# Performance work log

Hardware: AMD Instinct MI355X
Metric: run time of the kernel (lower is better)

Reference implementation:

```python
import jax, jax.numpy as jnp
import numpy as np

T = 100          # number of landscape sample points
K_MAX = 2        # landscape depth
GRID = (256, 256)
N = GRID[0] * GRID[1]
B = 256          # batch size
P = 1024         # persistence pairs per sample (from the cubical complex)
DIMENSIONS = (0, 1)
BIG = jnp.float32(1e30)  # finite sentinel instead of inf (avoids inf arithmetic)


def setup_inputs() -> dict:
    key = jax.random.key(0)
    k1, k2, k3, k4 = jax.random.split(key, 4)
    inputs = jax.random.uniform(k1, (B, N), dtype=jnp.float32)
    dim_idx = jax.random.randint(k2, (B, P), 0, 2, dtype=jnp.int32)
    b_loc = jax.random.randint(k3, (B, P), 0, N, dtype=jnp.int32)
    d_loc = jax.random.randint(k4, (B, P), 0, N, dtype=jnp.int32)
    # persistence pairs satisfy death value >= birth value; swap to honor that
    vb = jnp.take_along_axis(inputs, b_loc, axis=1)
    vd = jnp.take_along_axis(inputs, d_loc, axis=1)
    swap = vb > vd
    birth_loc = jnp.where(swap, d_loc, b_loc)
    death_loc = jnp.where(swap, b_loc, d_loc)
    return {"inputs": inputs, "dim_idx": dim_idx,
            "birth_loc": birth_loc, "death_loc": death_loc}


def _landscape_sample(dtm, dim_idx, b_loc, d_loc):
    # dtm: [N] filtration values; pairs: [P] each
    births = dtm[b_loc]  # [P] birth value = input at birth cell
    deaths = dtm[d_loc]  # [P]
    lands, trange = [], []
    for dim in DIMENSIONS:
        valid = dim_idx == dim                     # [P] pairs of this homology dim
        count = jnp.sum(valid)
        # robust t-range: first K_MAX valid pairs in given (lexsort) order
        rank = jnp.cumsum(valid.astype(jnp.int32)) - 1
        sel = valid & (rank < K_MAX)
        t_min = jnp.min(jnp.where(sel, births, BIG))
        t_max = jnp.max(jnp.where(sel, deaths, -BIG))
        t_min = jnp.where(count > 0, t_min, 0.0)
        t_max = jnp.where(count > 0, t_max, 0.0)
        # original custom grad does NOT differentiate through tseq
        tseq = jax.lax.stop_gradient(jnp.linspace(t_min, t_max, T))  # [T]
        b = jnp.where(valid, births, BIG)
        d = jnp.where(valid, deaths, -BIG)
        # tent functions: [T, P]
        fab = jnp.maximum(jnp.minimum(tseq[:, None] - b[None, :],
                                      d[None, :] - tseq[:, None]), 0.0)
        land, _ = jax.lax.top_k(fab, K_MAX)        # == -sort(-fab)[:, :K_MAX]
        land = jnp.where(count > 0, land, jnp.zeros_like(land))
        nonzero = (count > 0) & (jnp.max(land) > 0)
        trange.append(jnp.where(nonzero, t_min, 0.0))
        trange.append(jnp.where(nonzero, t_max, 0.0))
        lands.append(land)
    return jnp.stack(lands), jax.lax.stop_gradient(jnp.stack(trange))


def reference(inputs, dim_idx, birth_loc, death_loc):
    # landscape: [B, len(DIMENSIONS), T, K_MAX]; t_range: [B, 2*len(DIMENSIONS)]
    land, t_range = jax.vmap(_landscape_sample)(inputs, dim_idx, birth_loc, death_loc)
    return land, t_range
```

## Files before the change

kernel.cpp:

```cpp
#include <hip/hip_runtime.h>

#define TT 100
#define PP 1024
#define NN 65536
#define BIGV 1e30f

__global__ __launch_bounds__(1024, 8) void adpl_kernel(
    const float* __restrict__ inputs,
    const int*   __restrict__ dim_idx,
    const int*   __restrict__ birth_loc,
    const int*   __restrict__ death_loc,
    float*       __restrict__ out_land,
    float*       __restrict__ out_trange)
{
    __shared__ float2 bd[PP];
    __shared__ unsigned long long s_mask[16];
    __shared__ float  s_tmin, s_tmax;
    __shared__ int    s_count;
    __shared__ int    s_maxland;
    __shared__ float2 s_part[TT][9];

    const int b   = blockIdx.x;
    const int d   = blockIdx.y;
    const int tid = threadIdx.x;

    if (tid == 0) s_maxland = 0;

    {
        const int p  = tid;
        const int di = dim_idx [(size_t)b * PP + p];
        const int bl = birth_loc[(size_t)b * PP + p];
        const int dl = death_loc[(size_t)b * PP + p];
        const float bv = inputs[(size_t)b * NN + bl];
        const float dv = inputs[(size_t)b * NN + dl];
        const bool v = (di == d);
        bd[p] = v ? make_float2(bv, dv) : make_float2(BIGV, -BIGV);
        const unsigned long long m = __ballot(v);
        if ((tid & 63) == 0) s_mask[tid >> 6] = m;
    }
    __syncthreads();

    if (tid == 0) {
        int cnt = 0, p1 = -1, p2 = -1;
        for (int w = 0; w < 16; w++) {
            unsigned long long m = s_mask[w];
            cnt += __popcll(m);
            if (p2 < 0 && m) {
                if (p1 < 0) {
                    p1 = w * 64 + __ffsll(m) - 1;
                    m &= m - 1;
                    if (m) p2 = w * 64 + __ffsll(m) - 1;
                } else {
                    p2 = w * 64 + __ffsll(m) - 1;
                }
            }
        }
        float tmin = 0.f, tmax = 0.f;
        if (cnt > 0) {
            const float2 e1 = bd[p1];
            tmin = e1.x; tmax = e1.y;
            if (cnt > 1) {
                const float2 e2 = bd[p2];
                tmin = fminf(tmin, e2.x);
                tmax = fmaxf(tmax, e2.y);
            }
        }
        s_tmin = tmin; s_tmax = tmax; s_count = cnt;
    }
    __syncthreads();

    {
        const int t = tid >> 3;
        const int c = tid & 7;
        if (t < TT) {
            const float tmin = s_tmin, tmax = s_tmax;
            const float step = (tmax - tmin) * (1.0f / (TT - 1));
            const float tv = (t == TT - 1) ? tmax : fmaf((float)t, step, tmin);
            float M1 = 0.f, M2 = 0.f;
            #pragma unroll 8
            for (int i = 0; i < 128; i++) {
                const float2 e = bd[8 * i + c];
                const float f = fminf(tv - e.x, e.y - tv);
                M2 = fmaxf(M2, fminf(M1, f));
                M1 = fmaxf(M1, f);
            }
            s_part[t][c] = make_float2(M1, M2);
        }
    }
    __syncthreads();

    if (tid < TT) {
        const int t = tid;
        float m1 = 0.f, m2 = 0.f;
        #pragma unroll
        for (int cc = 0; cc < 8; cc++) {
            const float2 pr = s_part[t][cc];
            m2 = fmaxf(m2, fminf(m1, pr.x));
            m1 = fmaxf(m1, pr.x);
            m2 = fmaxf(m2, pr.y);
        }
        const size_t base = ((size_t)(b * 2 + d) * TT + t) * 2;
        out_land[base + 0] = m1;
        out_land[base + 1] = m2;
        atomicMax(&s_maxland, __float_as_int(m1));
    }
    __syncthreads();

    if (tid == 0) {
        const bool nz = (s_count > 0) && (__int_as_float(s_maxland) > 0.f);
        out_trange[(size_t)b * 4 + 2 * d + 0] = nz ? s_tmin : 0.f;
        out_trange[(size_t)b * 4 + 2 * d + 1] = nz ? s_tmax : 0.f;
    }
}

extern "C" void kernel_launch(void* const* d_in, const int* in_sizes, int n_in,
                              void* d_out, int out_size, void* d_ws, size_t ws_size,
                              hipStream_t stream) {
    const float* inputs    = (const float*)d_in[0];
    const int*   dim_idx   = (const int*)d_in[1];
    const int*   birth_loc = (const int*)d_in[2];
    const int*   death_loc = (const int*)d_in[3];

    const int B = in_sizes[1] / PP;

    float* out_land   = (float*)d_out;
    float* out_trange = out_land + (size_t)B * 2 * TT * 2;

    dim3 grid(B, 2);
    adpl_kernel<<<grid, 1024, 0, stream>>>(inputs, dim_idx, birth_loc, death_loc,
                                           out_land, out_trange);
}
```

Measured before the change: 105.4 us.

## Register-block four t-values per thread and predicate gathers on dimension match

The tent-function top-2 pass is remapped so each thread handles 4 sample points across 32 pair lanes instead of 1 point across 8 lanes. Each shared-memory pair load is now reused four times, and the final reduction grows to 32 partials per t. Birth and death locations and input values are only gathered for pairs whose dimension matches, which roughly halves scattered global reads. Output stores are vectorised to float2. In exchange, only 800 threads do the main loop and the reduction is longer.

```diff
diff --git a/kernel.cpp b/kernel.cpp
--- a/kernel.cpp
+++ b/kernel.cpp
@@ -18,7 +18,7 @@
     __shared__ float  s_tmin, s_tmax;
     __shared__ int    s_count;
     __shared__ int    s_maxland;
-    __shared__ float2 s_part[TT][9];
+    __shared__ float2 s_part[TT][33];
 
     const int b   = blockIdx.x;
     const int d   = blockIdx.y;
@@ -28,13 +28,16 @@
 
     {
         const int p  = tid;
-        const int di = dim_idx [(size_t)b * PP + p];
-        const int bl = birth_loc[(size_t)b * PP + p];
-        const int dl = death_loc[(size_t)b * PP + p];
-        const float bv = inputs[(size_t)b * NN + bl];
-        const float dv = inputs[(size_t)b * NN + dl];
+        const int di = dim_idx[(size_t)b * PP + p];
         const bool v = (di == d);
-        bd[p] = v ? make_float2(bv, dv) : make_float2(BIGV, -BIGV);
+        float bv = BIGV, dv = -BIGV;
+        if (v) {
+            const int bl = birth_loc[(size_t)b * PP + p];
+            const int dl = death_loc[(size_t)b * PP + p];
+            bv = inputs[(size_t)b * NN + bl];
+            dv = inputs[(size_t)b * NN + dl];
+        }
+        bd[p] = make_float2(bv, dv);
         const unsigned long long m = __ballot(v);
         if ((tid & 63) == 0) s_mask[tid >> 6] = m;
     }
@@ -69,47 +72,55 @@
     }
     __syncthreads();
 
-    {
-        const int t = tid >> 3;
-        const int c = tid & 7;
-        if (t < TT) {
-            const float tmin = s_tmin, tmax = s_tmax;
-            const float step = (tmax - tmin) * (1.0f / (TT - 1));
-            const float tv = (t == TT - 1) ? tmax : fmaf((float)t, step, tmin);
-            float M1 = 0.f, M2 = 0.f;
-            #pragma unroll 8
-            for (int i = 0; i < 128; i++) {
-                const float2 e = bd[8 * i + c];
-                const float f = fminf(tv - e.x, e.y - tv);
-                M2 = fmaxf(M2, fminf(M1, f));
-                M1 = fmaxf(M1, f);
+    if (tid < 800) {
+        const int tg = tid >> 5;
+        const int c  = tid & 31;
+        const float tmin = s_tmin, tmax = s_tmax;
+        const float step = (tmax - tmin) * (1.0f / (TT - 1));
+        float tv[4], m1[4], m2[4];
+        #pragma unroll
+        for (int j = 0; j < 4; j++) {
+            const int t = 4 * tg + j;
+            tv[j] = (t == TT - 1) ? tmax : fmaf((float)t, step, tmin);
+            m1[j] = 0.f; m2[j] = 0.f;
+        }
+        #pragma unroll 8
+        for (int i = 0; i < 32; i++) {
+            const float2 e = bd[32 * i + c];
+            #pragma unroll
+            for (int j = 0; j < 4; j++) {
+                const float f = fminf(tv[j] - e.x, e.y - tv[j]);
+                m2[j] = fmaxf(m2[j], fminf(m1[j], f));
+                m1[j] = fmaxf(m1[j], f);
             }
-            s_part[t][c] = make_float2(M1, M2);
         }
+        #pragma unroll
+        for (int j = 0; j < 4; j++)
+            s_part[4 * tg + j][c] = make_float2(m1[j], m2[j]);
     }
     __syncthreads();
 
     if (tid < TT) {
         const int t = tid;
         float m1 = 0.f, m2 = 0.f;
-        #pragma unroll
-        for (int cc = 0; cc < 8; cc++) {
-            const float2 pr = s_part[t][cc];
-            m2 = fmaxf(m2, fminf(m1, pr.x));
+        #pragma unroll 8
+        for (int c = 0; c < 32; c++) {
+            const float2 pr = s_part[t][c];
+            m2 = fmaxf(fminf(m1, pr.x), fmaxf(m2, pr.y));
             m1 = fmaxf(m1, pr.x);
-            m2 = fmaxf(m2, pr.y);
         }
         const size_t base = ((size_t)(b * 2 + d) * TT + t) * 2;
-        out_land[base + 0] = m1;
-        out_land[base + 1] = m2;
+        *reinterpret_cast<float2*>(out_land + base) = make_float2(m1, m2);
         atomicMax(&s_maxland, __float_as_int(m1));
     }
     __syncthreads();
 
     if (tid == 0) {
         const bool nz = (s_count > 0) && (__int_as_float(s_maxland) > 0.f);
-        out_trange[(size_t)b * 4 + 2 * d + 0] = nz ? s_tmin : 0.f;
-        out_trange[(size_t)b * 4 + 2 * d + 1] = nz ? s_tmax : 0.f;
+        const float tmn = nz ? s_tmin : 0.f;
+        const float tmx = nz ? s_tmax : 0.f;
+        *reinterpret_cast<float2*>(out_trange + (size_t)b * 4 + 2 * d) =
+            make_float2(tmn, tmx);
     }
 }
 
```

Result: no change. 106.6 us (+1.2%).
